# Kernel tuning notes

Measured on AMD Instinct MI355X. Metric: run time of the kernel, lower is better.

Reference implementation:

```python
import jax, jax.numpy as jnp
import numpy as np

B, T, ENC_H, DEC_H, ATTN = 128, 2048, 512, 512, 128


def setup_inputs() -> dict:
    key = jax.random.key(0)
    k1, k2, k3, k4, k5 = jax.random.split(key, 5)
    s = lambda fan_in: 1.0 / np.sqrt(fan_in)
    return {
        "encoder_outputs": jax.random.normal(k1, (B, T, ENC_H), dtype=jnp.float32),
        "decoder_hidden": jax.random.normal(k2, (B, DEC_H), dtype=jnp.float32),
        # nn.Linear weights are [out_features, in_features]
        "W_enc": jax.random.uniform(k3, (ATTN, ENC_H), jnp.float32, -s(ENC_H), s(ENC_H)),
        "W_dec": jax.random.uniform(k4, (ATTN, DEC_H), jnp.float32, -s(DEC_H), s(DEC_H)),
        "v_w": jax.random.uniform(k5, (1, ATTN), jnp.float32, -s(ATTN), s(ATTN)),
    }


def reference(encoder_outputs, decoder_hidden, W_enc, W_dec, v_w):
    # enc_proj: [B, T, A]
    enc_proj = jnp.einsum("bth,ah->bta", encoder_outputs, W_enc)
    # dec_proj: [B, 1, A]
    dec_proj = jnp.einsum("bh,ah->ba", decoder_hidden, W_dec)[:, None, :]
    energy = jnp.tanh(enc_proj + dec_proj)                      # [B, T, A]
    scores = jnp.einsum("bta,a->bt", energy, v_w[0])            # [B, T]
    weights = jax.nn.softmax(scores, axis=-1)                   # [B, T]
    context = jnp.einsum("bt,bth->bh", weights, encoder_outputs)  # [B, ENC_H]
    return context, weights
```

## Files before the change

### kernel.cpp

```cpp
#include <hip/hip_runtime.h>
#include <hip/hip_bf16.h>

#define B_SZ   128
#define T_SZ   2048
#define ENCH   512
#define ATTN_  128
#define NBLK   256
#define SEGS_PER_BLK 4

typedef __attribute__((ext_vector_type(8))) short short8;
typedef __attribute__((ext_vector_type(4))) float f32x4;

__device__ __forceinline__ unsigned short f2bf_rne(float f) {
  unsigned u = __builtin_bit_cast(unsigned, f);
  u += 0x7FFFu + ((u >> 16) & 1u);
  return (unsigned short)(u >> 16);
}
__device__ __forceinline__ float fast_tanh(float x) {
  float e = __expf(2.f * x);
  return 1.f - __fdividef(2.f, e + 1.f);
}
__device__ __forceinline__ short8 pack8(float4 a, float4 b) {
  union { unsigned u[4]; short8 s; } r;
  asm("v_cvt_pk_bf16_f32 %0, %1, %2" : "=v"(r.u[0]) : "v"(a.x), "v"(a.y));
  asm("v_cvt_pk_bf16_f32 %0, %1, %2" : "=v"(r.u[1]) : "v"(a.z), "v"(a.w));
  asm("v_cvt_pk_bf16_f32 %0, %1, %2" : "=v"(r.u[2]) : "v"(b.x), "v"(b.y));
  asm("v_cvt_pk_bf16_f32 %0, %1, %2" : "=v"(r.u[3]) : "v"(b.z), "v"(b.w));
  return r.s;
}
template<int CTRL>
__device__ __forceinline__ float dpp_add(float v) {
  int t = __builtin_amdgcn_update_dpp(0, __builtin_bit_cast(int, v),
                                      CTRL, 0xf, 0xf, true);
  return v + __builtin_bit_cast(float, t);
}
__device__ __forceinline__ float sum16(float v) {
  v = dpp_add<0xB1>(v);
  v = dpp_add<0x4E>(v);
  v = dpp_add<0x141>(v);
  v = dpp_add<0x140>(v);
  return v;
}
__device__ __forceinline__ float bfel(short8 v, int j_half, bool hi) {
  unsigned u = __builtin_bit_cast(unsigned, (int)((((int*)&v))[j_half]));
  return __builtin_bit_cast(float, hi ? (u & 0xFFFF0000u) : (u << 16));
}

__global__ void k_prep(const float* __restrict__ w,
                       unsigned short* __restrict__ o,
                       const float* __restrict__ dec,
                       const float* __restrict__ wdec,
                       float* __restrict__ dout) {
  if (blockIdx.x < 32) {
    int idx = blockIdx.x * 256 + threadIdx.x;
    int l   = idx & 63;
    int wks = idx >> 6;
    int cg  = wks >> 4, ks = wks & 15;
    int row = cg * 16 + (l & 15);
    int col = ks * 32 + (l >> 4) * 8;
    const float4* src = reinterpret_cast<const float4*>(w + row * ENCH + col);
    float4 v0 = src[0], v1 = src[1];
    short8 r;
    r[0] = (short)f2bf_rne(v0.x); r[1] = (short)f2bf_rne(v0.y);
    r[2] = (short)f2bf_rne(v0.z); r[3] = (short)f2bf_rne(v0.w);
    r[4] = (short)f2bf_rne(v1.x); r[5] = (short)f2bf_rne(v1.y);
    r[6] = (short)f2bf_rne(v1.z); r[7] = (short)f2bf_rne(v1.w);
    *reinterpret_cast<short8*>(o + (size_t)idx * 8) = r;
  } else {
    __shared__ float dh[ENCH];
    int b = blockIdx.x - 32, tid = threadIdx.x;
    for (int i = tid; i < ENCH; i += 256) dh[i] = dec[b * ENCH + i];
    __syncthreads();
    if (tid < 128) {
      const float4* wr4 = reinterpret_cast<const float4*>(wdec + tid * ENCH);
      float acc = 0.f;
      for (int h4 = 0; h4 < ENCH / 4; ++h4) {
        float4 w4 = wr4[h4];
        acc += dh[h4 * 4 + 0] * w4.x + dh[h4 * 4 + 1] * w4.y +
               dh[h4 * 4 + 2] * w4.z + dh[h4 * 4 + 3] * w4.w;
      }
      dout[b * ATTN_ + tid] = acc;
    }
  }
}

__global__ __launch_bounds__(1024, 4) void k_main(
    const float* __restrict__ enc,
    const unsigned short* __restrict__ wfrag,
    const float* __restrict__ decproj,
    const float* __restrict__ vw,
    float* __restrict__ scores_raw,
    float* __restrict__ ctx_part,
    float* __restrict__ ml_part)
{
  const int tid  = threadIdx.x;
  const int lane = tid & 63;
  const int wid  = tid >> 6;
  const int l15  = lane & 15;
  const int g    = lane >> 4;

  __shared__ unsigned short w_lds[ATTN_ * ENCH];
  __shared__ float dv_lds[ATTN_], vv_lds[ATTN_];

  const int b    = blockIdx.x >> 1;
  const int seg0 = (blockIdx.x & 1) * 4;

#pragma unroll
  for (int r = 0; r < 8; ++r) {
    int i = r * 1024 + tid;
    reinterpret_cast<short8*>(w_lds)[i] = reinterpret_cast<const short8*>(wfrag)[i];
  }
  if (tid < 128)       dv_lds[tid] = decproj[b * ATTN_ + tid];
  else if (tid < 256)  vv_lds[tid - 128] = vw[tid - 128];
  __syncthreads();

#pragma unroll 1
  for (int k = 0; k < wid; ++k) __builtin_amdgcn_s_sleep(6);

#pragma unroll 1
  for (int i = 0; i < SEGS_PER_BLK; ++i) {
    const int seg  = seg0 + i;
    const int row0 = seg * 256 + wid * 16;
    const float* arow = enc + ((size_t)b * T_SZ + row0 + l15) * ENCH + g * 8;

    short8 af[16];
#pragma unroll
    for (int ks = 0; ks < 16; ++ks) {
      float4 a0 = *reinterpret_cast<const float4*>(arow + ks * 32);
      float4 a1 = *reinterpret_cast<const float4*>(arow + ks * 32 + 4);
      af[ks] = pack8(a0, a1);
    }

    float e[4] = {0.f, 0.f, 0.f, 0.f};
#pragma unroll 1
    for (int half = 0; half < 2; ++half) {
      f32x4 acc[4];
#pragma unroll
      for (int c = 0; c < 4; ++c) acc[c] = (f32x4){0.f, 0.f, 0.f, 0.f};
#pragma unroll
      for (int ks = 0; ks < 16; ++ks) {
        const char* wb = (const char*)w_lds + ks * 1024 + lane * 16 + half * 65536;
#pragma unroll
        for (int c = 0; c < 4; ++c) {
          short8 bf = *reinterpret_cast<const short8*>(wb + c * 16384);
          acc[c] = __builtin_amdgcn_mfma_f32_16x16x32_bf16(af[ks], bf, acc[c], 0, 0, 0);
        }
      }
#pragma unroll
      for (int c = 0; c < 4; ++c) {
        int col = (half * 4 + c) * 16 + l15;
        float d = dv_lds[col], v = vv_lds[col];
#pragma unroll
        for (int r = 0; r < 4; ++r)
          e[r] += fast_tanh(acc[c][r] + d) * v;
      }
    }

    float er[4];
#pragma unroll
    for (int r = 0; r < 4; ++r) er[r] = sum16(e[r]);
    if (l15 == 0) {
#pragma unroll
      for (int r = 0; r < 4; ++r)
        scores_raw[(size_t)b * T_SZ + row0 + g * 4 + r] = er[r];
    }

    float mg = fmaxf(fmaxf(er[0], er[1]), fmaxf(er[2], er[3]));
    mg = fmaxf(mg, __shfl_xor(mg, 16));
    mg = fmaxf(mg, __shfl_xor(mg, 32));
    float x0 = __expf(er[0] - mg), x1 = __expf(er[1] - mg);
    float x2 = __expf(er[2] - mg), x3 = __expf(er[3] - mg);
    float xs = (x0 + x1) + (x2 + x3);
    xs += __shfl_xor(xs, 16);
    xs += __shfl_xor(xs, 32);
    const float l_run = xs;
    float sel = (l15 & 3) == 0 ? er[0]
              : (l15 & 3) == 1 ? er[1]
              : (l15 & 3) == 2 ? er[2] : er[3];
    float smine = __shfl(sel, ((l15 >> 2) << 4) | (l15 & 3));
    const float p_me = __expf(smine - mg);

    float ctx8[8];
#pragma unroll
    for (int j = 0; j < 8; ++j) ctx8[j] = 0.f;
#pragma unroll
    for (int ks = 0; ks < 16; ++ks) {
      float c[8];
#pragma unroll
      for (int jh = 0; jh < 4; ++jh) {
        c[jh * 2 + 0] = p_me * bfel(af[ks], jh, false);
        c[jh * 2 + 1] = p_me * bfel(af[ks], jh, true);
      }
#pragma unroll
      for (int j = 0; j < 8; ++j) c[j] = sum16(c[j]);
      if (l15 == ks) {
#pragma unroll
        for (int j = 0; j < 8; ++j) ctx8[j] = c[j];
      }
    }

    const size_t widx = (size_t)b * 128 + seg * 16 + wid;
    float* cp = ctx_part + widx * ENCH + l15 * 32 + g * 8;
    *reinterpret_cast<float4*>(cp)     = (float4){ctx8[0], ctx8[1], ctx8[2], ctx8[3]};
    *reinterpret_cast<float4*>(cp + 4) = (float4){ctx8[4], ctx8[5], ctx8[6], ctx8[7]};
    if (lane == 0) {
      ml_part[widx * 2 + 0] = mg;
      ml_part[widx * 2 + 1] = l_run;
    }
  }
}

__global__ void k_combine(const float* __restrict__ ctx_part,
                          const float* __restrict__ ml_part,
                          float* __restrict__ out_ctx,
                          float* __restrict__ weights)
{
  __shared__ float msh[128], lsh[128], fac[128];
  int b = blockIdx.x, tid = threadIdx.x;
  if (tid < 128) {
    msh[tid] = ml_part[((size_t)b * 128 + tid) * 2 + 0];
    lsh[tid] = ml_part[((size_t)b * 128 + tid) * 2 + 1];
  }
  __syncthreads();
  float M = msh[0];
  for (int w = 1; w < 128; ++w) M = fmaxf(M, msh[w]);
  if (tid < 128) fac[tid] = __expf(msh[tid] - M);
  __syncthreads();
  float L = 0.f;
  for (int w = 0; w < 128; ++w) L += fac[w] * lsh[w];
  float Linv = 1.f / L;
  for (int h = tid; h < ENCH; h += 256) {
    float a = 0.f;
    for (int w = 0; w < 128; ++w)
      a += fac[w] * ctx_part[((size_t)b * 128 + w) * ENCH + h];
    out_ctx[b * ENCH + h] = a * Linv;
  }
  for (int t = tid; t < T_SZ; t += 256) {
    float raw = weights[(size_t)b * T_SZ + t];
    weights[(size_t)b * T_SZ + t] = __expf(raw - M) * Linv;
  }
}

extern "C" void kernel_launch(void* const* d_in, const int* in_sizes, int n_in,
                              void* d_out, int out_size, void* d_ws, size_t ws_size,
                              hipStream_t stream) {
  const float* enc  = (const float*)d_in[0];
  const float* dec  = (const float*)d_in[1];
  const float* wenc = (const float*)d_in[2];
  const float* wdec = (const float*)d_in[3];
  const float* vw   = (const float*)d_in[4];

  float* out     = (float*)d_out;
  float* out_ctx = out;
  float* out_w   = out + B_SZ * ENCH;

  char* ws = (char*)d_ws;
  unsigned short* wfrag = (unsigned short*)ws;
  float* decproj  = (float*)(ws + 131072);
  float* ml_part  = (float*)(ws + 131072 + 65536);
  float* ctx_part = (float*)(ws + 131072 + 65536 + 131072);

  hipLaunchKernelGGL(k_prep, dim3(160), dim3(256), 0, stream,
                     wenc, wfrag, dec, wdec, decproj);
  hipLaunchKernelGGL(k_main, dim3(NBLK), dim3(1024), 0, stream,
                     enc, wfrag, decproj, vw, out_w, ctx_part, ml_part);
  hipLaunchKernelGGL(k_combine, dim3(B_SZ), dim3(256), 0, stream,
                     ctx_part, ml_part, out_ctx, out_w);
}
```

Baseline: 167.7 us.

## Merge flash-softmax partials in registers and LDS before writing to global

```diff
diff --git a/kernel.cpp b/kernel.cpp
--- a/kernel.cpp
+++ b/kernel.cpp
@@ -117,6 +117,11 @@
 #pragma unroll 1
   for (int k = 0; k < wid; ++k) __builtin_amdgcn_s_sleep(6);
 
+  float m_run = -INFINITY, l_run = 0.f;
+  float ctx8[8];
+#pragma unroll
+  for (int j = 0; j < 8; ++j) ctx8[j] = 0.f;
+
 #pragma unroll 1
   for (int i = 0; i < SEGS_PER_BLK; ++i) {
     const int seg  = seg0 + i;
@@ -173,16 +178,15 @@
     float xs = (x0 + x1) + (x2 + x3);
     xs += __shfl_xor(xs, 16);
     xs += __shfl_xor(xs, 32);
-    const float l_run = xs;
     float sel = (l15 & 3) == 0 ? er[0]
               : (l15 & 3) == 1 ? er[1]
               : (l15 & 3) == 2 ? er[2] : er[3];
     float smine = __shfl(sel, ((l15 >> 2) << 4) | (l15 & 3));
     const float p_me = __expf(smine - mg);
 
-    float ctx8[8];
-#pragma unroll
-    for (int j = 0; j < 8; ++j) ctx8[j] = 0.f;
+    float cseg[8];
+#pragma unroll
+    for (int j = 0; j < 8; ++j) cseg[j] = 0.f;
 #pragma unroll
     for (int ks = 0; ks < 16; ++ks) {
       float c[8];
@@ -195,17 +199,43 @@
       for (int j = 0; j < 8; ++j) c[j] = sum16(c[j]);
       if (l15 == ks) {
 #pragma unroll
-        for (int j = 0; j < 8; ++j) ctx8[j] = c[j];
-      }
-    }
-
-    const size_t widx = (size_t)b * 128 + seg * 16 + wid;
-    float* cp = ctx_part + widx * ENCH + l15 * 32 + g * 8;
-    *reinterpret_cast<float4*>(cp)     = (float4){ctx8[0], ctx8[1], ctx8[2], ctx8[3]};
-    *reinterpret_cast<float4*>(cp + 4) = (float4){ctx8[4], ctx8[5], ctx8[6], ctx8[7]};
-    if (lane == 0) {
-      ml_part[widx * 2 + 0] = mg;
-      ml_part[widx * 2 + 1] = l_run;
+        for (int j = 0; j < 8; ++j) cseg[j] = c[j];
+      }
+    }
+
+    float m_new  = fmaxf(m_run, mg);
+    float scale  = __expf(m_run - m_new);
+    float fseg   = __expf(mg - m_new);
+    l_run = l_run * scale + xs * fseg;
+#pragma unroll
+    for (int j = 0; j < 8; ++j) ctx8[j] = ctx8[j] * scale + cseg[j] * fseg;
+    m_run = m_new;
+  }
+
+  __syncthreads();
+  float* cred = reinterpret_cast<float*>(w_lds);
+  float* cp = cred + wid * ENCH + l15 * 32 + g * 8;
+#pragma unroll
+  for (int j = 0; j < 8; ++j) cp[j] = ctx8[j];
+  if (lane == 0) { dv_lds[wid * 2] = m_run; dv_lds[wid * 2 + 1] = l_run; }
+  __syncthreads();
+
+  if (tid < ENCH) {
+    float M = dv_lds[0];
+#pragma unroll
+    for (int w = 1; w < 16; ++w) M = fmaxf(M, dv_lds[w * 2]);
+    float L = 0.f, c = 0.f;
+#pragma unroll
+    for (int w = 0; w < 16; ++w) {
+      float f = __expf(dv_lds[w * 2] - M);
+      L += f * dv_lds[w * 2 + 1];
+      c += f * cred[w * ENCH + tid];
+    }
+    const int widx2 = b * 2 + (blockIdx.x & 1);
+    ctx_part[(size_t)widx2 * ENCH + tid] = c;
+    if (tid == 0) {
+      ml_part[widx2 * 2 + 0] = M;
+      ml_part[widx2 * 2 + 1] = L;
     }
   }
 }
@@ -215,24 +245,20 @@
                           float* __restrict__ out_ctx,
                           float* __restrict__ weights)
 {
-  __shared__ float msh[128], lsh[128], fac[128];
+  __shared__ float f0s, f1s, Msh, Lsh;
   int b = blockIdx.x, tid = threadIdx.x;
-  if (tid < 128) {
-    msh[tid] = ml_part[((size_t)b * 128 + tid) * 2 + 0];
-    lsh[tid] = ml_part[((size_t)b * 128 + tid) * 2 + 1];
-  }
-  __syncthreads();
-  float M = msh[0];
-  for (int w = 1; w < 128; ++w) M = fmaxf(M, msh[w]);
-  if (tid < 128) fac[tid] = __expf(msh[tid] - M);
-  __syncthreads();
-  float L = 0.f;
-  for (int w = 0; w < 128; ++w) L += fac[w] * lsh[w];
-  float Linv = 1.f / L;
+  if (tid == 0) {
+    float m0 = ml_part[b * 4 + 0], l0 = ml_part[b * 4 + 1];
+    float m1 = ml_part[b * 4 + 2], l1 = ml_part[b * 4 + 3];
+    float M  = fmaxf(m0, m1);
+    float f0 = __expf(m0 - M), f1 = __expf(m1 - M);
+    Msh = M; Lsh = f0 * l0 + f1 * l1; f0s = f0; f1s = f1;
+  }
+  __syncthreads();
+  float M = Msh, Linv = 1.f / Lsh, f0 = f0s, f1 = f1s;
   for (int h = tid; h < ENCH; h += 256) {
-    float a = 0.f;
-    for (int w = 0; w < 128; ++w)
-      a += fac[w] * ctx_part[((size_t)b * 128 + w) * ENCH + h];
+    float a = f0 * ctx_part[(size_t)(b * 2) * ENCH + h] +
+              f1 * ctx_part[(size_t)(b * 2 + 1) * ENCH + h];
     out_ctx[b * ENCH + h] = a * Linv;
   }
   for (int t = tid; t < T_SZ; t += 256) {
@@ -258,7 +284,7 @@
   unsigned short* wfrag = (unsigned short*)ws;
   float* decproj  = (float*)(ws + 131072);
   float* ml_part  = (float*)(ws + 131072 + 65536);
-  float* ctx_part = (float*)(ws + 131072 + 65536 + 131072);
+  float* ctx_part = (float*)(ws + 131072 + 65536 + 2048);
 
   hipLaunchKernelGGL(k_prep, dim3(160), dim3(256), 0, stream,
                      wenc, wfrag, dec, wdec, decproj);
```

Result: faster. 148.4 us, median of 2 (-11.5%).
